# Kernel tuning notes

Measured on AMD Instinct MI355X. Metric: run time of the kernel, lower is better.

The kernel has to match this reference:

```python
import jax, jax.numpy as jnp
import numpy as np

N_NODES = 100000
N_EDGES = 1600000
D = 64


def setup_inputs() -> dict:
    key = jax.random.key(0)
    ks = jax.random.split(key, 9)
    x = jax.random.normal(ks[0], (N_NODES, D), dtype=jnp.float32)
    edge_index = jax.random.randint(ks[1], (2, N_EDGES), 0, N_NODES, dtype=jnp.int64)
    W_self = jax.random.normal(ks[2], (D, D), dtype=jnp.float32) * (D ** -0.5)
    b_self = jax.random.normal(ks[3], (D,), dtype=jnp.float32) * 0.01
    W_neigh = jax.random.normal(ks[4], (D, D), dtype=jnp.float32) * (D ** -0.5)
    b_neigh = jax.random.normal(ks[5], (D,), dtype=jnp.float32) * 0.01
    W_var = jax.random.normal(ks[6], (D, D), dtype=jnp.float32) * (D ** -0.5)
    b_var = jax.random.normal(ks[7], (D,), dtype=jnp.float32) * 0.01
    return {"x": x, "edge_index": edge_index, "W_self": W_self, "b_self": b_self,
            "W_neigh": W_neigh, "b_neigh": b_neigh, "W_var": W_var, "b_var": b_var}


def reference(x, edge_index, W_self, b_self, W_neigh, b_neigh, W_var, b_var):
    N, d = x.shape
    scale = d ** -0.5
    src, dst = edge_index[0], edge_index[1]

    x_src = x[src]                                   # [E, d]
    x_dst = x[dst]                                   # [E, d]

    # reciprocal attention: scatter_softmax over incoming edges of dst
    logits = jnp.sum(x_src * x_dst, axis=-1) * scale               # [E]
    seg_max = jax.ops.segment_max(logits, dst, num_segments=N)     # [N]
    ex = jnp.exp(logits - seg_max[dst])                            # [E]
    denom = jax.ops.segment_sum(ex, dst, num_segments=N)           # [N]
    attn = ex / denom[dst]                                         # [E]

    msg = jax.ops.segment_sum(x_src * attn[:, None], dst, num_segments=N)  # [N, d]

    out = x @ W_self.T + b_self + msg @ W_neigh.T + b_neigh

    # variance via double scatter_mean
    cnt = jax.ops.segment_sum(jnp.ones_like(logits), dst, num_segments=N)
    cnt = jnp.maximum(cnt, 1.0)[:, None]                           # [N, 1]
    msg_mean = jax.ops.segment_sum(x_src, dst, num_segments=N) / cnt
    diff_sq = (x_src - msg_mean[dst]) ** 2                         # [E, d]
    var = jax.ops.segment_sum(diff_sq, dst, num_segments=N) / cnt  # [N, d]

    out = out + var @ W_var.T + b_var
    return out
```

## Files before the change

### kernel.cpp

```cpp
#include <hip/hip_runtime.h>


static inline size_t ws_align(size_t x) { return (x + 255) & ~size_t(255); }

typedef __attribute__((ext_vector_type(8))) short bf16x8;
typedef __attribute__((ext_vector_type(4))) float f32x4;
typedef __attribute__((ext_vector_type(2))) float f32x2;

#define ECHUNK 4096

__device__ __forceinline__ unsigned short f2bf(float f) {
    unsigned u = __builtin_bit_cast(unsigned, f);
    u += 0x7FFFu + ((u >> 16) & 1u);
    return (unsigned short)(u >> 16);
}
__device__ __forceinline__ float bfhi(int d) {
    return __builtin_bit_cast(float, (unsigned)d & 0xFFFF0000u);
}
__device__ __forceinline__ float bflo(int d) {
    return __builtin_bit_cast(float, (unsigned)d << 16);
}

#define EXP_SCALE 0.18033688f
__device__ __forceinline__ float fast_exp8(float t) {
#if __has_builtin(__builtin_amdgcn_exp2f)
    return __builtin_amdgcn_exp2f(t * EXP_SCALE);
#else
    return __expf(t * 0.125f);
#endif
}

__global__ void __launch_bounds__(256) hist_cast_kernel(
        const float* __restrict__ x, unsigned short* __restrict__ xb,
        const int* __restrict__ ei, int* __restrict__ hist,
        int E, int n4, int nblk, int nb1) {
    __shared__ int h[512];
    for (int k = threadIdx.x; k < nb1; k += 256) h[k] = 0;
    int stride = gridDim.x * 256;
    for (int i = blockIdx.x * 256 + threadIdx.x; i < n4; i += stride) {
        float4 v = ((const float4*)x)[i];
        ushort4 hh; hh.x = f2bf(v.x); hh.y = f2bf(v.y); hh.z = f2bf(v.z); hh.w = f2bf(v.w);
        ((ushort4*)xb)[i] = hh;
    }
    __syncthreads();
    const int* dstp = ei + E;
    int base = blockIdx.x * ECHUNK;
    #pragma unroll 4
    for (int k = 0; k < ECHUNK / 256; ++k) {
        int e = base + k * 256 + threadIdx.x;
        if (e < E) atomicAdd(&h[dstp[e] >> 8], 1);
    }
    __syncthreads();
    for (int k = threadIdx.x; k < nb1; k += 256) hist[k * nblk + blockIdx.x] = h[k];
}

__global__ void scan_a_kernel(int* __restrict__ h, int* __restrict__ bsum, int M) {
    __shared__ int t[256];
    int i = blockIdx.x * 256 + threadIdx.x;
    int v = (i < M) ? h[i] : 0;
    t[threadIdx.x] = v;
    __syncthreads();
    for (int off = 1; off < 256; off <<= 1) {
        int u = (threadIdx.x >= (unsigned)off) ? t[threadIdx.x - off] : 0;
        __syncthreads();
        t[threadIdx.x] += u;
        __syncthreads();
    }
    if (i < M) h[i] = t[threadIdx.x] - v;
    if (threadIdx.x == 255) bsum[blockIdx.x] = t[255];
}

__global__ void scan_b_kernel(int* __restrict__ bsum, int nb) {
    __shared__ int t[1024];
    int i = threadIdx.x;
    int v = (i < nb) ? bsum[i] : 0;
    t[i] = v;
    __syncthreads();
    for (int off = 1; off < 1024; off <<= 1) {
        int u = (i >= off) ? t[i - off] : 0;
        __syncthreads();
        t[i] += u;
        __syncthreads();
    }
    if (i < nb) bsum[i] = t[i] - v;
}

__global__ void __launch_bounds__(256) part_kernel(
        const int* __restrict__ ei, const int* __restrict__ offs,
        const int* __restrict__ bsum, int* __restrict__ tmp,
        int E, int nblk, int nb1) {
    __shared__ int lofs[512];
    int b = blockIdx.x;
    for (int k = threadIdx.x; k < nb1; k += 256) {
        int idx = k * nblk + b;
        lofs[k] = offs[idx] + bsum[idx >> 8];
    }
    __syncthreads();
    const int* dstp = ei + E;
    int base = b * ECHUNK;
    #pragma unroll 4
    for (int k = 0; k < ECHUNK / 256; ++k) {
        int e = base + k * 256 + threadIdx.x;
        if (e < E) {
            int dst = dstp[e];
            int src = ei[e];
            int pos = atomicAdd(&lofs[dst >> 8], 1);
            tmp[pos] = (src << 8) | (dst & 255);
        }
    }
}

__global__ void __launch_bounds__(256) fsort_kernel(
        const int* __restrict__ tmp, const int* __restrict__ offs,
        const int* __restrict__ bsum, int* __restrict__ srcs,
        int* __restrict__ rs, int E, int N, int nblk, int nb1) {
    __shared__ int cnt[256], sc[256], lofs[256];
    int b = blockIdx.x, tid = threadIdx.x;
    int i0 = b * nblk;
    int start = offs[i0] + bsum[i0 >> 8];
    int end;
    if (b == nb1 - 1) end = E;
    else { int i1 = (b + 1) * nblk; end = offs[i1] + bsum[i1 >> 8]; }

    cnt[tid] = 0;
    __syncthreads();
    for (int e = start + tid; e < end; e += 256) atomicAdd(&cnt[tmp[e] & 255], 1);
    __syncthreads();
    int c = cnt[tid];
    sc[tid] = c;
    __syncthreads();
    for (int off = 1; off < 256; off <<= 1) {
        int u = (tid >= off) ? sc[tid - off] : 0;
        __syncthreads();
        sc[tid] += u;
        __syncthreads();
    }
    int excl = sc[tid] - c;
    int node = b * 256 + tid;
    if (node < N) rs[node] = start + excl;
    lofs[tid] = start + excl;
    __syncthreads();
    for (int e = start + tid; e < end; e += 256) {
        int v = tmp[e];
        int pos = atomicAdd(&lofs[v & 255], 1);
        srcs[pos] = v >> 8;
    }
    if (b == 0 && tid == 0) rs[N] = E;
}

__global__ void __launch_bounds__(256) node_gather_kernel(
        const unsigned short* __restrict__ xb,
        const int* __restrict__ rs, const int* __restrict__ srcs,
        unsigned short* __restrict__ msgvar, int N) {
    int w = (blockIdx.x * blockDim.x + threadIdx.x) >> 6;
    if (w >= N) return;
    int lane = threadIdx.x & 63;
    int q = lane & 15;
    int g = lane >> 4;
    int s = rs[w], e = rs[w + 1];
    const int2* xb2 = (const int2*)xb;
    int2 dn = xb2[(size_t)w * 16 + q];
    f32x2 xn01 = {bflo(dn.x), bfhi(dn.x)}, xn23 = {bflo(dn.y), bfhi(dn.y)};
    float den = 0.f;
    f32x2 sxa = {0,0}, sxb = {0,0}, ssqa = {0,0}, ssqb = {0,0},
          smea = {0,0}, smeb = {0,0};

    auto compute = [&](int2 d) {
        f32x2 a = {bflo(d.x), bfhi(d.x)};
        f32x2 b = {bflo(d.y), bfhi(d.y)};
        f32x2 dp = a * xn01 + b * xn23;
        float t = dp.x + dp.y;
        #pragma unroll
        for (int off = 1; off < 16; off <<= 1) t += __shfl_xor(t, off, 64);
        float ex = fast_exp8(t);
        f32x2 ex2 = {ex, ex};
        den += ex;
        sxa += a;           sxb += b;
        ssqa += a * a;      ssqb += b * b;
        smea += ex2 * a;    smeb += ex2 * b;
    };

    for (int base = s; base < e; base += 64) {
        int cnt = min(e - base, 64);
        int idx = srcs[base + min(lane, cnt - 1)];
        int p = 0;
        int2 da, db;
        if (p + 8 <= cnt) {
            int ra = __shfl(idx, p + g, 64);
            int rb = __shfl(idx, p + 4 + g, 64);
            da = xb2[(size_t)ra * 16 + q];
            db = xb2[(size_t)rb * 16 + q];
        }
        for (; p + 16 <= cnt; p += 8) {
            int ra1 = __shfl(idx, p + 8 + g, 64);
            int rb1 = __shfl(idx, p + 12 + g, 64);
            int2 da1 = xb2[(size_t)ra1 * 16 + q];
            int2 db1 = xb2[(size_t)rb1 * 16 + q];
            compute(da);
            compute(db);
            da = da1; db = db1;
        }
        if (p + 8 <= cnt) {
            compute(da);
            compute(db);
            p += 8;
        }
        if (p + 4 <= cnt) {
            int r = __shfl(idx, p + g, 64);
            compute(xb2[(size_t)r * 16 + q]);
            p += 4;
        }
        if (p < cnt) {
            float wt = (p + g < cnt) ? 1.f : 0.f;
            int r = __shfl(idx, min(p + g, cnt - 1), 64);
            int2 d = xb2[(size_t)r * 16 + q];
            f32x2 a = {bflo(d.x), bfhi(d.x)};
            f32x2 b = {bflo(d.y), bfhi(d.y)};
            f32x2 dp = a * xn01 + b * xn23;
            float t = dp.x + dp.y;
            #pragma unroll
            for (int off = 1; off < 16; off <<= 1) t += __shfl_xor(t, off, 64);
            float ex = fast_exp8(t) * wt;
            f32x2 wt2 = {wt, wt}, ex2 = {ex, ex};
            f32x2 wa = a * wt2, wb = b * wt2;
            den += ex;
            sxa += wa;          sxb += wb;
            ssqa += wa * a;     ssqb += wb * b;
            smea += ex2 * a;    smeb += ex2 * b;
        }
    }
    #pragma unroll
    for (int off = 16; off < 64; off <<= 1) {
        den    += __shfl_xor(den,    off, 64);
        sxa.x  += __shfl_xor(sxa.x,  off, 64); sxa.y  += __shfl_xor(sxa.y,  off, 64);
        sxb.x  += __shfl_xor(sxb.x,  off, 64); sxb.y  += __shfl_xor(sxb.y,  off, 64);
        ssqa.x += __shfl_xor(ssqa.x, off, 64); ssqa.y += __shfl_xor(ssqa.y, off, 64);
        ssqb.x += __shfl_xor(ssqb.x, off, 64); ssqb.y += __shfl_xor(ssqb.y, off, 64);
        smea.x += __shfl_xor(smea.x, off, 64); smea.y += __shfl_xor(smea.y, off, 64);
        smeb.x += __shfl_xor(smeb.x, off, 64); smeb.y += __shfl_xor(smeb.y, off, 64);
    }
    if (lane < 16) {
        float inv = 1.f / fmaxf((float)(e - s), 1.f);
        float invden = (den > 0.f) ? (1.f / den) : 0.f;
        float m0 = sxa.x * inv, m1 = sxa.y * inv, m2 = sxb.x * inv, m3 = sxb.y * inv;
        ushort4 hm, hv;
        hm.x = f2bf(smea.x * invden); hm.y = f2bf(smea.y * invden);
        hm.z = f2bf(smeb.x * invden); hm.w = f2bf(smeb.y * invden);
        hv.x = f2bf(ssqa.x * inv - m0 * m0); hv.y = f2bf(ssqa.y * inv - m1 * m1);
        hv.z = f2bf(ssqb.x * inv - m2 * m2); hv.w = f2bf(ssqb.y * inv - m3 * m3);
        *(ushort4*)&msgvar[(size_t)w * 128 + 4 * q]      = hm;
        *(ushort4*)&msgvar[(size_t)w * 128 + 64 + 4 * q] = hv;
    }
}

__global__ void __launch_bounds__(256) gemm_kernel(
        const unsigned short* __restrict__ xb, const unsigned short* __restrict__ msgvar,
        const float* __restrict__ Ws, const float* __restrict__ bs,
        const float* __restrict__ Wn, const float* __restrict__ bn,
        const float* __restrict__ Wv, const float* __restrict__ bv,
        float* __restrict__ out, int N) {
    __shared__ unsigned short As[64 * 200];
    int tid = threadIdx.x;
    int lane = tid & 63;
    int wv = tid >> 6;
    int j = lane & 15, quad = lane >> 4;
    int jg = wv * 16 + j;

    const float* Wm0[3] = {Ws, Wn, Wv};
    bf16x8 bfrag[6];
    #pragma unroll
    for (int ks = 0; ks < 6; ++ks) {
        const float* W = Wm0[ks >> 1];
        int k0 = (ks & 1) * 32 + quad * 8;
        const float4* p = (const float4*)(W + (size_t)jg * 64 + k0);
        float4 a = p[0], b = p[1];
        bf16x8 f;
        f[0] = (short)f2bf(a.x); f[1] = (short)f2bf(a.y);
        f[2] = (short)f2bf(a.z); f[3] = (short)f2bf(a.w);
        f[4] = (short)f2bf(b.x); f[5] = (short)f2bf(b.y);
        f[6] = (short)f2bf(b.z); f[7] = (short)f2bf(b.w);
        bfrag[ks] = f;
    }
    float bias = bs[jg] + bn[jg] + bv[jg];

    #pragma unroll
    for (int t = 0; t < 2; ++t) {
        int nbase = blockIdx.x * 128 + t * 64;
        #pragma unroll
        for (int i = 0; i < 4; ++i) {
            int idx = i * 256 + tid;
            int row = idx >> 4, c = idx & 15;
            int n = min(nbase + row, N - 1);
            ushort4 h = ((const ushort4*)(xb + (size_t)n * 64))[c];
            *(ushort4*)&As[row * 200 + c * 4] = h;
        }
        #pragma unroll
        for (int i = 0; i < 8; ++i) {
            int idx = i * 256 + tid;
            int row = idx >> 5, c = idx & 31;
            int n = min(nbase + row, N - 1);
            ushort4 h = ((const ushort4*)(msgvar + (size_t)n * 128))[c];
            *(ushort4*)&As[row * 200 + 64 + c * 4] = h;
        }
        __syncthreads();

        f32x4 acc[4];
        #pragma unroll
        for (int nt = 0; nt < 4; ++nt) {
            acc[nt][0] = bias; acc[nt][1] = bias; acc[nt][2] = bias; acc[nt][3] = bias;
        }
        #pragma unroll
        for (int nt = 0; nt < 4; ++nt) {
            #pragma unroll
            for (int ks = 0; ks < 6; ++ks) {
                const bf16x8* ap = (const bf16x8*)&As[(nt * 16 + j) * 200 + ks * 32 + quad * 8];
                acc[nt] = __builtin_amdgcn_mfma_f32_16x16x32_bf16(*ap, bfrag[ks], acc[nt], 0, 0, 0);
            }
        }
        #pragma unroll
        for (int nt = 0; nt < 4; ++nt) {
            #pragma unroll
            for (int r = 0; r < 4; ++r) {
                int node = nbase + nt * 16 + quad * 4 + r;
                if (node < N) out[(size_t)node * 64 + jg] = acc[nt][r];
            }
        }
        __syncthreads();
    }
}

extern "C" void kernel_launch(void* const* d_in, const int* in_sizes, int n_in,
                              void* d_out, int out_size, void* d_ws, size_t ws_size,
                              hipStream_t stream) {
    const float* x  = (const float*)d_in[0];
    const int*   ei = (const int*)d_in[1];
    const float* Ws = (const float*)d_in[2];
    const float* bs = (const float*)d_in[3];
    const float* Wn = (const float*)d_in[4];
    const float* bn = (const float*)d_in[5];
    const float* Wv = (const float*)d_in[6];
    const float* bv = (const float*)d_in[7];
    float* out = (float*)d_out;

    int N  = in_sizes[0] / 64;
    int E  = in_sizes[1] / 2;
    int nblk = (E + ECHUNK - 1) / ECHUNK;
    int nb1  = (N + 255) >> 8;
    int M    = nb1 * nblk;
    int NBs  = (M + 255) / 256;

    char* wsp = (char*)d_ws;
    size_t off = 0;
    int* hist   = (int*)(wsp + off); off += ws_align((size_t)M * 4);
    int* bsumi  = (int*)(wsp + off); off += ws_align((size_t)NBs * 4);
    int* rs     = (int*)(wsp + off); off += ws_align((size_t)(N + 1) * 4);
    int* tmp    = (int*)(wsp + off); off += ws_align((size_t)E * 4);
    int* srcs   = (int*)(wsp + off); off += ws_align((size_t)E * 4);
    unsigned short* msgvar = (unsigned short*)(wsp + off); off += ws_align((size_t)N * 128 * 2);
    unsigned short* xb     = (unsigned short*)(wsp + off); off += ws_align((size_t)N * 64 * 2);

    int n4 = N * 16;
    hist_cast_kernel<<<nblk, 256, 0, stream>>>(x, xb, ei, hist, E, n4, nblk, nb1);
    scan_a_kernel<<<NBs, 256, 0, stream>>>(hist, bsumi, M);
    scan_b_kernel<<<1, 1024, 0, stream>>>(bsumi, NBs);
    part_kernel<<<nblk, 256, 0, stream>>>(ei, hist, bsumi, tmp, E, nblk, nb1);
    fsort_kernel<<<nb1, 256, 0, stream>>>(tmp, hist, bsumi, srcs, rs, E, N, nblk, nb1);
    node_gather_kernel<<<((size_t)N * 64 + 255) / 256, 256, 0, stream>>>(xb, rs, srcs, msgvar, N);
    gemm_kernel<<<(N + 127) / 128, 256, 0, stream>>>(xb, msgvar, Ws, bs, Wn, bn, Wv, bv, out, N);
}
```

Measured before the change: 219.2 us.

## Use DPP row reductions for edge logits and halve edge chunk size

Replaces the 16-lane shuffle-xor dot-product reduction with DPP row operations (quad_perm swaps plus row_shr by 4 and 8), which avoids LDS-backed ds_bpermute traffic in the per-edge inner loop. It also halves the edge chunk per block in the histogram and partition kernels, doubling the block count, and makes the second-level scan loop over more than 1024 block sums, since the larger block count can exceed one tile. The exp is switched back to __expf with a 0.125 scale, removing the hand-folded exp2 constant.

```diff
diff --git a/kernel.cpp b/kernel.cpp
--- a/kernel.cpp
+++ b/kernel.cpp
@@ -7,7 +7,7 @@
 typedef __attribute__((ext_vector_type(4))) float f32x4;
 typedef __attribute__((ext_vector_type(2))) float f32x2;
 
-#define ECHUNK 4096
+#define ECHUNK 2048
 
 __device__ __forceinline__ unsigned short f2bf(float f) {
     unsigned u = __builtin_bit_cast(unsigned, f);
@@ -21,13 +21,18 @@
     return __builtin_bit_cast(float, (unsigned)d << 16);
 }
 
-#define EXP_SCALE 0.18033688f
-__device__ __forceinline__ float fast_exp8(float t) {
-#if __has_builtin(__builtin_amdgcn_exp2f)
-    return __builtin_amdgcn_exp2f(t * EXP_SCALE);
-#else
-    return __expf(t * 0.125f);
-#endif
+template <int CTRL>
+__device__ __forceinline__ float dpp_radd(float t) {
+    int v = __builtin_amdgcn_update_dpp(0, __builtin_bit_cast(int, t),
+                                        CTRL, 0xF, 0xF, true);
+    return t + __builtin_bit_cast(float, v);
+}
+__device__ __forceinline__ float row16_sum(float t) {
+    t = dpp_radd<0xB1>(t);
+    t = dpp_radd<0x4E>(t);
+    t = dpp_radd<0x124>(t);
+    t = dpp_radd<0x128>(t);
+    return t;
 }
 
 __global__ void __launch_bounds__(256) hist_cast_kernel(
@@ -72,17 +77,26 @@
 
 __global__ void scan_b_kernel(int* __restrict__ bsum, int nb) {
     __shared__ int t[1024];
-    int i = threadIdx.x;
-    int v = (i < nb) ? bsum[i] : 0;
-    t[i] = v;
-    __syncthreads();
-    for (int off = 1; off < 1024; off <<= 1) {
-        int u = (i >= off) ? t[i - off] : 0;
-        __syncthreads();
-        t[i] += u;
-        __syncthreads();
-    }
-    if (i < nb) bsum[i] = t[i] - v;
+    __shared__ int carry;
+    if (threadIdx.x == 0) carry = 0;
+    __syncthreads();
+    for (int base = 0; base < nb; base += 1024) {
+        int i = base + threadIdx.x;
+        int v = (i < nb) ? bsum[i] : 0;
+        t[threadIdx.x] = v;
+        __syncthreads();
+        for (int off = 1; off < 1024; off <<= 1) {
+            int u = (threadIdx.x >= off) ? t[threadIdx.x - off] : 0;
+            __syncthreads();
+            t[threadIdx.x] += u;
+            __syncthreads();
+        }
+        int c = carry;
+        if (i < nb) bsum[i] = t[threadIdx.x] - v + c;
+        __syncthreads();
+        if (threadIdx.x == 1023) carry = c + t[1023];
+        __syncthreads();
+    }
 }
 
 __global__ void __launch_bounds__(256) part_kernel(
@@ -169,10 +183,8 @@
         f32x2 a = {bflo(d.x), bfhi(d.x)};
         f32x2 b = {bflo(d.y), bfhi(d.y)};
         f32x2 dp = a * xn01 + b * xn23;
-        float t = dp.x + dp.y;
-        #pragma unroll
-        for (int off = 1; off < 16; off <<= 1) t += __shfl_xor(t, off, 64);
-        float ex = fast_exp8(t);
+        float t = row16_sum(dp.x + dp.y);
+        float ex = __expf(t * 0.125f);
         f32x2 ex2 = {ex, ex};
         den += ex;
         sxa += a;           sxb += b;
@@ -217,10 +229,8 @@
             f32x2 a = {bflo(d.x), bfhi(d.x)};
             f32x2 b = {bflo(d.y), bfhi(d.y)};
             f32x2 dp = a * xn01 + b * xn23;
-            float t = dp.x + dp.y;
-            #pragma unroll
-            for (int off = 1; off < 16; off <<= 1) t += __shfl_xor(t, off, 64);
-            float ex = fast_exp8(t) * wt;
+            float t = row16_sum(dp.x + dp.y);
+            float ex = __expf(t * 0.125f) * wt;
             f32x2 wt2 = {wt, wt}, ex2 = {ex, ex};
             f32x2 wa = a * wt2, wb = b * wt2;
             den += ex;
```

New measurement: 207.3 us. -5.4%, faster.
